# Performance work log

Measured on AMD Instinct MI355X. Metric: run time of the kernel, lower is better.

Reference implementation:

```python
import jax, jax.numpy as jnp
import numpy as np

H, N, RANK = 256, 64, 1
SEQ_L = 8192


def setup_inputs() -> dict:
    key = jax.random.key(0)
    ks = jax.random.split(key, 12)
    # timescales dt in [1e-3, 1e-1] -> log_dt uniform in [log 1e-3, log 1e-1]
    log_dt = jax.random.uniform(ks[0], (H,), jnp.float32,
                                minval=np.log(1e-3), maxval=np.log(1e-1))
    def cplx(kr, ki, shape, scale=1.0):
        return (scale * jax.random.normal(kr, shape, jnp.float32),
                scale * jax.random.normal(ki, shape, jnp.float32))
    C_re, C_im = cplx(ks[1], ks[2], (1, H, N))
    B_re, B_im = cplx(ks[3], ks[4], (1, H, N))
    P_re, P_im = cplx(ks[5], ks[6], (RANK, H, N), scale=0.5)
    Q_re, Q_im = cplx(ks[7], ks[8], (RANK, H, N), scale=0.5)
    # HiPPO-NPLR-like poles: Re(w) < 0 (Hurwitz), Im(w) = pi*n ladder
    w_re = -(0.5 + 0.5 * jax.random.uniform(ks[9], (H, N), jnp.float32))
    w_im = jnp.broadcast_to(np.pi * jnp.arange(N, dtype=jnp.float32), (H, N))
    return {
        "log_dt": log_dt,
        "C_re": C_re, "C_im": C_im,
        "B_re": B_re, "B_im": B_im,
        "P_re": P_re, "P_im": P_im,
        "Q_re": Q_re, "Q_im": Q_im,
        "w_re": w_re, "w_im": w_im,
        "L": SEQ_L,
    }


def reference(log_dt, C_re, C_im, B_re, B_im, P_re, P_im, Q_re, Q_im,
              w_re, w_im, L):
    # SSKernelNPLR.forward with rate=1.0, state=None, rank=1.
    Lf = L // 2 + 1
    dt = jnp.exp(log_dt)                                   # (H,)
    w = (w_re + 1j * w_im).astype(jnp.complex64)           # (H, N)
    B = (B_re + 1j * B_im).astype(jnp.complex64)           # (1, H, N)
    C = (C_re + 1j * C_im).astype(jnp.complex64)           # (1, H, N)
    P = (P_re + 1j * P_im).astype(jnp.complex64)           # (r, H, N)
    Q = (Q_re + 1j * Q_im).astype(jnp.complex64)           # (r, H, N)

    # bilinear-transform FFT nodes
    omega = jnp.exp((-2j * jnp.pi / L) * jnp.arange(Lf)).astype(jnp.complex64)  # (Lf,)
    z = 2.0 * (1.0 - omega) / (1.0 + omega)                # (Lf,)

    wdt = w * dt[:, None]                                  # (H, N)
    Bc = jnp.concatenate([B, P], axis=0)                   # (1+r, H, N)
    Cc = jnp.concatenate([C, Q], axis=0)                   # (1+r, H, N)
    v = Bc[None, :, :, :] * Cc[:, None, :, :]              # (1+r, 1+r, H, N)

    # Cauchy kernel: r[a,b,h,l] = sum_n v[a,b,h,n] / (z[l] - wdt[h,n])
    recip = 1.0 / (z[None, None, :] - wdt[:, :, None])     # (H, N, Lf)
    r = jnp.einsum('abhn,hnl->abhl', v, recip)             # (1+r, 1+r, H, Lf)
    r = r * dt[None, None, :, None]

    # rank-1 Woodbury correction
    k_f = r[:1, :1] - r[:1, 1:] * r[1:, :1] / (1.0 + r[1:, 1:])  # (1, 1, H, Lf)
    k_f = k_f * 2.0 / (1.0 + omega)

    k = jnp.fft.irfft(k_f, n=L, axis=-1)[..., :L]          # (1, 1, H, L) real
    k_B = k[-1]                                            # (1, H, L)
    return k_B
```

## Files before the change

### kernel.cpp

```cpp
#include <hip/hip_runtime.h>
#include <hip/hip_fp16.h>
#include <math.h>

#define HDIM 256
#define NDIM 64
#define LDIM 8192
#define LF   4097
#define MDIM 4096
#define LOG2M 12
#define TWN  2048

typedef _Float16 f16x8 __attribute__((ext_vector_type(8)));
typedef float    f32x4 __attribute__((ext_vector_type(4)));

__device__ __forceinline__ int cvt_pk_f16(float lo, float hi) {
    union { __half2 h; int i; } u;
    u.h = __floats2half2_rn(lo, hi);
    return u.i;
}

__device__ __forceinline__ int swz(int i) {
    return i ^ (((i >> 4) ^ (i >> 8)) & 15);
}

__global__ __launch_bounds__(1024, 4) void fused_kernel(
    const float* __restrict__ log_dt,
    const float* __restrict__ C_re, const float* __restrict__ C_im,
    const float* __restrict__ B_re, const float* __restrict__ B_im,
    const float* __restrict__ P_re, const float* __restrict__ P_im,
    const float* __restrict__ Q_re, const float* __restrict__ Q_im,
    const float* __restrict__ w_re, const float* __restrict__ w_im,
    float2* __restrict__ out2)
{
    __shared__ float2 S[MDIM + 1];
    __shared__ float2 TW[TWN];

    const int h    = blockIdx.x;
    const int tid  = threadIdx.x;
    const int lane = tid & 63;
    const int wave = tid >> 6;
    const int g    = lane >> 4;
    const int m    = lane & 15;
    const float dt = expf(log_dt[h]);
    const float dtM = dt * (1.f / (float)MDIM);
    const int hb   = h * NDIM;

    {
        float s, c;
        sincosf((3.14159265358979323846f / (float)TWN) * (float)tid, &s, &c);
        TW[swz(tid)] = make_float2(c, s);
        sincosf((3.14159265358979323846f / (float)TWN) * (float)(tid + 1024), &s, &c);
        TW[swz(tid + 1024)] = make_float2(c, s);
    }

    if (tid < 64) {
        const float br = B_re[hb + lane], bi = B_im[hb + lane];
        const float cr = C_re[hb + lane], ci = C_im[hb + lane];
        float sr = cr * br - ci * bi;
        float si = cr * bi + ci * br;
        #pragma unroll
        for (int off = 32; off > 0; off >>= 1) {
            sr += __shfl_xor(sr, off);
            si += __shfl_xor(si, off);
        }
        if (tid == 0)
            S[swz(MDIM)] = make_float2(0.5f * dtM * sr, 0.5f * dtM * si);
    }

    float nwr_[16], nw2_[16], wi_[16];
    int   av[4][4];
    {
        const bool arow = (m < 8);
        const int  ai   = m >> 1;
        const int  c    = m & 1;
        const float* fre = (ai >= 2) ? Q_re : C_re;
        const float* fim = (ai >= 2) ? Q_im : C_im;
        const float* sre = (ai & 1) ? P_re : B_re;
        const float* sim = (ai & 1) ? P_im : B_im;
        #pragma unroll
        for (int q = 0; q < 4; ++q) {
            #pragma unroll
            for (int t = 0; t < 4; ++t) {
                const int n = hb + 16 * q + 4 * g + t;
                const float nw = -w_re[n] * dt;
                nwr_[q * 4 + t] = nw;
                nw2_[q * 4 + t] = nw * nw;
                wi_[q * 4 + t]  = w_im[n] * dt;
                float e0 = 0.f, e1 = 0.f;
                if (arow) {
                    const float fr = fre[n], fi = fim[n];
                    const float s2r = sre[n], s2i = sim[n];
                    const float vr = fr * s2r - fi * s2i;
                    const float vi = fr * s2i + fi * s2r;
                    e0 = c ? vi : vr;
                    e1 = c ? vr : -vi;
                }
                av[q][t] = cvt_pk_f16(e0, e1);
            }
        }
    }

    const int lbase = wave * 256 + m;

    float zt_[16];
    {
        float ch, sh;
        const float a0 = (3.14159265358979323846f / (float)LDIM) * (float)lbase;
        sincosf(a0, &sh, &ch);
        const float cd = 0.99998117528260114265f;
        const float sd = 0.00613588464915447536f;
        #pragma unroll
        for (int t16 = 0; t16 < 16; ++t16) {
            zt_[t16] = 2.f * sh * __builtin_amdgcn_rcpf(ch);
            const float chn = ch * cd - sh * sd;
            const float shn = sh * cd + ch * sd;
            ch = chn; sh = shn;
        }
    }

    #pragma unroll 4
    for (int t16 = 0; t16 < 16; ++t16) {
        const float zt = zt_[t16];

        f32x4 acc0 = {0.f, 0.f, 0.f, 0.f};
        f32x4 acc1 = {0.f, 0.f, 0.f, 0.f};
        #pragma unroll
        for (int q = 0; q < 4; ++q) {
            float den[4], tim[4];
            #pragma unroll
            for (int t = 0; t < 4; ++t) {
                tim[t] = zt - wi_[q * 4 + t];
                den[t] = fmaf(tim[t], tim[t], nw2_[q * 4 + t]);
            }
            const float p01 = den[0] * den[1];
            const float p23 = den[2] * den[3];
            const float rp01 = __builtin_amdgcn_rcpf(p01);
            const float rp23 = __builtin_amdgcn_rcpf(p23);
            const float rc0 = rp01 * den[1], rc1 = rp01 * den[0];
            const float rc2 = rp23 * den[3], rc3 = rp23 * den[2];

            int bv[4];
            bv[0] = cvt_pk_f16(nwr_[q * 4 + 0] * rc0, -(tim[0] * rc0));
            bv[1] = cvt_pk_f16(nwr_[q * 4 + 1] * rc1, -(tim[1] * rc1));
            bv[2] = cvt_pk_f16(nwr_[q * 4 + 2] * rc2, -(tim[2] * rc2));
            bv[3] = cvt_pk_f16(nwr_[q * 4 + 3] * rc3, -(tim[3] * rc3));

            union { int i[4]; f16x8 v; } ua, ub;
            ua.i[0] = av[q][0]; ua.i[1] = av[q][1];
            ua.i[2] = av[q][2]; ua.i[3] = av[q][3];
            ub.i[0] = bv[0]; ub.i[1] = bv[1]; ub.i[2] = bv[2]; ub.i[3] = bv[3];
            if (q < 2)
                acc0 = __builtin_amdgcn_mfma_f32_16x16x32_f16(ua.v, ub.v, acc0, 0, 0, 0);
            else
                acc1 = __builtin_amdgcn_mfma_f32_16x16x32_f16(ua.v, ub.v, acc1, 0, 0, 0);
        }
        const f32x4 acc = acc0 + acc1;

        const float o0 = __shfl_xor(acc[0], 16);
        const float o1 = __shfl_xor(acc[1], 16);
        const float o2 = __shfl_xor(acc[2], 16);
        const float o3 = __shfl_xor(acc[3], 16);
        if (lane < 16) {
            const int l = lbase + t16 * 16;
            const float numr = acc[2] * o0 - acc[3] * o1;
            const float numi = acc[2] * o1 + acc[3] * o0;
            const float d_r  = 1.f + dt * o2;
            const float d_i  = dt * o3;
            const float dd   = fmaf(d_r, d_r, d_i * d_i);
            const float rr2  = __builtin_amdgcn_rcpf(dd);
            const float cr = dt * ((numr * d_r + numi * d_i) * rr2);
            const float ci = dt * ((numi * d_r - numr * d_i) * rr2);
            const float Tr = acc[0] - cr;
            const float Ti = acc[1] - ci;
            const float Ei = 0.5f * dtM * zt;
            S[swz(l)] = make_float2(dtM * Tr - Ei * Ti, dtM * Ti + Ei * Tr);
        }
    }

    __syncthreads();

    const int l0 = tid;
    const int l1 = tid + 1024;
    const float2 Kl0 = S[swz(l0)];
    const float2 Km0 = S[swz(MDIM - l0)];
    const float2 Kl1 = S[swz(l1)];
    const float2 Km1 = S[swz(MDIM - l1)];
    float2 K2;
    if (tid == 0) K2 = S[swz(2048)];

    float w0s, w0c;
    sincosf((3.14159265358979323846f / (float)MDIM) * (float)l0, &w0s, &w0c);
    const float r2 = 0.70710678118654752440f;
    const float w1c = (w0c - w0s) * r2;
    const float w1s = (w0s + w0c) * r2;

    __syncthreads();

    {
        const float Ar = 0.5f * (Kl0.x + Km0.x);
        const float Ai = 0.5f * (Kl0.y - Km0.y);
        const float Br = 0.5f * (Kl0.x - Km0.x);
        const float Bi = 0.5f * (Kl0.y + Km0.y);
        const float Or = w0c * Br - w0s * Bi;
        const float Oi = w0c * Bi + w0s * Br;
        const int bl = (int)(__brev((unsigned)l0) >> (32 - LOG2M));
        S[swz(bl)] = make_float2(Ar - Oi, Ai + Or);
        if (l0 > 0) {
            const int bm = (int)(__brev((unsigned)(MDIM - l0)) >> (32 - LOG2M));
            S[swz(bm)] = make_float2(Ar + Oi, Or - Ai);
        }
    }
    {
        const float Ar = 0.5f * (Kl1.x + Km1.x);
        const float Ai = 0.5f * (Kl1.y - Km1.y);
        const float Br = 0.5f * (Kl1.x - Km1.x);
        const float Bi = 0.5f * (Kl1.y + Km1.y);
        const float Or = w1c * Br - w1s * Bi;
        const float Oi = w1c * Bi + w1s * Br;
        const int bl = (int)(__brev((unsigned)l1) >> (32 - LOG2M));
        S[swz(bl)] = make_float2(Ar - Oi, Ai + Or);
        const int bm = (int)(__brev((unsigned)(MDIM - l1)) >> (32 - LOG2M));
        S[swz(bm)] = make_float2(Ar + Oi, Or - Ai);
    }
    if (tid == 0) {
        S[swz(1)] = make_float2(K2.x, -K2.y);
    }

    #pragma unroll
    for (int stage = 0; stage < LOG2M; ++stage) {
        const int half = 1 << stage;
        __syncthreads();
        #pragma unroll 2
        for (int t = tid; t < MDIM / 2; t += 1024) {
            const int pos = t & (half - 1);
            const int i0  = ((t & ~(half - 1)) << 1) | pos;
            const int i1  = i0 + half;
            const float2 w = TW[swz(pos << (LOG2M - 1 - stage))];
            const float2 a = S[swz(i0)];
            const float2 b = S[swz(i1)];
            const float tr = w.x * b.x - w.y * b.y;
            const float ti = w.x * b.y + w.y * b.x;
            S[swz(i0)] = make_float2(a.x + tr, a.y + ti);
            S[swz(i1)] = make_float2(a.x - tr, a.y - ti);
        }
    }
    __syncthreads();

    for (int n = tid; n < MDIM; n += 1024) {
        out2[(size_t)h * MDIM + n] = S[swz(n)];
    }
}

extern "C" void kernel_launch(void* const* d_in, const int* in_sizes, int n_in,
                              void* d_out, int out_size, void* d_ws, size_t ws_size,
                              hipStream_t stream)
{
    const float* log_dt = (const float*)d_in[0];
    const float* C_re   = (const float*)d_in[1];
    const float* C_im   = (const float*)d_in[2];
    const float* B_re   = (const float*)d_in[3];
    const float* B_im   = (const float*)d_in[4];
    const float* P_re   = (const float*)d_in[5];
    const float* P_im   = (const float*)d_in[6];
    const float* Q_re   = (const float*)d_in[7];
    const float* Q_im   = (const float*)d_in[8];
    const float* w_re   = (const float*)d_in[9];
    const float* w_im   = (const float*)d_in[10];

    float2* out2 = (float2*)d_out;

    fused_kernel<<<HDIM, 1024, 0, stream>>>(log_dt, C_re, C_im, B_re, B_im,
                                            P_re, P_im, Q_re, Q_im,
                                            w_re, w_im, out2);
}
```

Baseline: 37.39 us.

## Replace radix-2 shared-memory FFT with radix-4 stages and digit-reversed input

Rewrites the 4096-point inverse FFT from twelve radix-2 stages to six radix-4 stages. Each thread now handles one 4-point butterfly per stage, so there are half as many barriers and fewer LDS round trips. Inputs are scattered with base-4 digit reversal, and the twiddle table grows to 3072 entries. The cost is more sincos setup work, a larger shared twiddle table, and more registers per butterfly.

```diff
diff --git a/kernel.cpp b/kernel.cpp
--- a/kernel.cpp
+++ b/kernel.cpp
@@ -8,7 +8,7 @@
 #define LF   4097
 #define MDIM 4096
 #define LOG2M 12
-#define TWN  2048
+#define TW4N 3072
 
 typedef _Float16 f16x8 __attribute__((ext_vector_type(8)));
 typedef float    f32x4 __attribute__((ext_vector_type(4)));
@@ -21,6 +21,11 @@
 
 __device__ __forceinline__ int swz(int i) {
     return i ^ (((i >> 4) ^ (i >> 8)) & 15);
+}
+
+__device__ __forceinline__ int drev(unsigned x) {
+    unsigned y = __brev(x) >> (32 - LOG2M);
+    return (int)(((y & 0x555u) << 1) | ((y >> 1) & 0x555u));
 }
 
 __global__ __launch_bounds__(1024, 4) void fused_kernel(
@@ -33,7 +38,7 @@
     float2* __restrict__ out2)
 {
     __shared__ float2 S[MDIM + 1];
-    __shared__ float2 TW[TWN];
+    __shared__ float2 TW4[TW4N];
 
     const int h    = blockIdx.x;
     const int tid  = threadIdx.x;
@@ -45,12 +50,10 @@
     const float dtM = dt * (1.f / (float)MDIM);
     const int hb   = h * NDIM;
 
-    {
+    for (int p = tid; p < TW4N; p += 1024) {
         float s, c;
-        sincosf((3.14159265358979323846f / (float)TWN) * (float)tid, &s, &c);
-        TW[swz(tid)] = make_float2(c, s);
-        sincosf((3.14159265358979323846f / (float)TWN) * (float)(tid + 1024), &s, &c);
-        TW[swz(tid + 1024)] = make_float2(c, s);
+        sincosf((6.28318530717958647692f / 4096.f) * (float)p, &s, &c);
+        TW4[swz(p)] = make_float2(c, s);
     }
 
     if (tid < 64) {
@@ -203,11 +206,9 @@
         const float Bi = 0.5f * (Kl0.y + Km0.y);
         const float Or = w0c * Br - w0s * Bi;
         const float Oi = w0c * Bi + w0s * Br;
-        const int bl = (int)(__brev((unsigned)l0) >> (32 - LOG2M));
-        S[swz(bl)] = make_float2(Ar - Oi, Ai + Or);
+        S[swz(drev((unsigned)l0))] = make_float2(Ar - Oi, Ai + Or);
         if (l0 > 0) {
-            const int bm = (int)(__brev((unsigned)(MDIM - l0)) >> (32 - LOG2M));
-            S[swz(bm)] = make_float2(Ar + Oi, Or - Ai);
+            S[swz(drev((unsigned)(MDIM - l0)))] = make_float2(Ar + Oi, Or - Ai);
         }
     }
     {
@@ -217,32 +218,41 @@
         const float Bi = 0.5f * (Kl1.y + Km1.y);
         const float Or = w1c * Br - w1s * Bi;
         const float Oi = w1c * Bi + w1s * Br;
-        const int bl = (int)(__brev((unsigned)l1) >> (32 - LOG2M));
-        S[swz(bl)] = make_float2(Ar - Oi, Ai + Or);
-        const int bm = (int)(__brev((unsigned)(MDIM - l1)) >> (32 - LOG2M));
-        S[swz(bm)] = make_float2(Ar + Oi, Or - Ai);
+        S[swz(drev((unsigned)l1))] = make_float2(Ar - Oi, Ai + Or);
+        S[swz(drev((unsigned)(MDIM - l1)))] = make_float2(Ar + Oi, Or - Ai);
     }
     if (tid == 0) {
-        S[swz(1)] = make_float2(K2.x, -K2.y);
+        S[swz(drev(2048u))] = make_float2(K2.x, -K2.y);
     }
 
     #pragma unroll
-    for (int stage = 0; stage < LOG2M; ++stage) {
-        const int half = 1 << stage;
+    for (int stage = 0; stage < 6; ++stage) {
+        const int q = 1 << (2 * stage);
         __syncthreads();
-        #pragma unroll 2
-        for (int t = tid; t < MDIM / 2; t += 1024) {
-            const int pos = t & (half - 1);
-            const int i0  = ((t & ~(half - 1)) << 1) | pos;
-            const int i1  = i0 + half;
-            const float2 w = TW[swz(pos << (LOG2M - 1 - stage))];
-            const float2 a = S[swz(i0)];
-            const float2 b = S[swz(i1)];
-            const float tr = w.x * b.x - w.y * b.y;
-            const float ti = w.x * b.y + w.y * b.x;
-            S[swz(i0)] = make_float2(a.x + tr, a.y + ti);
-            S[swz(i1)] = make_float2(a.x - tr, a.y - ti);
-        }
+        const int pos  = tid & (q - 1);
+        const int base = ((tid & ~(q - 1)) << 2) | pos;
+        const int f    = pos * (1024 >> (2 * stage));
+        const float2 w1 = TW4[swz(f)];
+        const float2 w2 = TW4[swz(2 * f)];
+        const float2 w3 = TW4[swz(3 * f)];
+        const float2 x0 = S[swz(base)];
+        const float2 x1 = S[swz(base + q)];
+        const float2 x2 = S[swz(base + 2 * q)];
+        const float2 x3 = S[swz(base + 3 * q)];
+        const float a1r = w1.x * x1.x - w1.y * x1.y;
+        const float a1i = w1.x * x1.y + w1.y * x1.x;
+        const float a2r = w2.x * x2.x - w2.y * x2.y;
+        const float a2i = w2.x * x2.y + w2.y * x2.x;
+        const float a3r = w3.x * x3.x - w3.y * x3.y;
+        const float a3i = w3.x * x3.y + w3.y * x3.x;
+        const float t0r = x0.x + a2r, t0i = x0.y + a2i;
+        const float t1r = x0.x - a2r, t1i = x0.y - a2i;
+        const float t2r = a1r + a3r,  t2i = a1i + a3i;
+        const float t3r = a1r - a3r,  t3i = a1i - a3i;
+        S[swz(base)]         = make_float2(t0r + t2r, t0i + t2i);
+        S[swz(base + q)]     = make_float2(t1r - t3i, t1i + t3r);
+        S[swz(base + 2 * q)] = make_float2(t0r - t2r, t0i - t2i);
+        S[swz(base + 3 * q)] = make_float2(t1r + t3i, t1i - t3r);
     }
     __syncthreads();
 
```

After: 36.29 us (median of 2 runs). 1.03x faster.
